# Performance work log

Hardware: AMD Instinct MI355X
Metric: run time of the kernel (lower is better)

The kernel has to match this reference:

```python
import jax, jax.numpy as jnp
from jax import lax
import numpy as np

B, H0, W0, C = 2, 192, 192, 192
CH = C // 2            # channels per attention branch (window / stripe)
D = 4                  # blocks in the stage
WS = 8                 # window / stripe size
NHW = 4                # window-attention heads
NHS = 4                # stripe-attention heads
ADF = 2                # anchor down factor (avgpool)
MLP_RATIO = 4

def _rel_pos_index(ws):
    coords = np.stack(np.meshgrid(np.arange(ws), np.arange(ws), indexing="ij"))
    coords = coords.reshape(2, -1)
    rel = coords[:, :, None] - coords[:, None, :]
    rel = rel.transpose(1, 2, 0) + (ws - 1)
    return rel[..., 0] * (2 * ws - 1) + rel[..., 1]

REL_IDX = jnp.asarray(_rel_pos_index(WS))  # [N, N] into (2*WS-1)^2 table

def _swin_mask(H, W, ws, shift):
    img = np.zeros((H, W))
    cnt = 0
    for hs in (slice(0, -ws), slice(-ws, -shift), slice(-shift, None)):
        for wsl in (slice(0, -ws), slice(-ws, -shift), slice(-shift, None)):
            img[hs, wsl] = cnt
            cnt += 1
    win = img.reshape(H // ws, ws, W // ws, ws).transpose(0, 2, 1, 3).reshape(-1, ws * ws)
    diff = win[:, None, :] - win[:, :, None]
    return jnp.asarray(np.where(diff != 0, -100.0, 0.0), jnp.float32)

def _ln(x, g, b):
    mu = x.mean(-1, keepdims=True)
    var = x.var(-1, keepdims=True)
    return (x - mu) * lax.rsqrt(var + 1e-5) * g + b

def _window_attn(xw, H, W, shift, qkv_w, qkv_b, rpb):
    Bb, L, Cw = xw.shape
    h, dh, N = NHW, Cw // NHW, WS * WS
    x = xw.reshape(Bb, H, W, Cw)
    if shift:
        x = jnp.roll(x, (-shift, -shift), (1, 2))
    nH, nW = H // WS, W // WS
    xw_ = x.reshape(Bb, nH, WS, nW, WS, Cw).transpose(0, 1, 3, 2, 4, 5).reshape(-1, N, Cw)
    qkv = (xw_ @ qkv_w + qkv_b).reshape(-1, N, 3, h, dh)
    q, k, v = qkv[:, :, 0], qkv[:, :, 1], qkv[:, :, 2]
    attn = jnp.einsum("wnhd,wmhd->whnm", q * dh ** -0.5, k)
    attn = attn + rpb[REL_IDX].transpose(2, 0, 1)[None]  # relative position bias [h,N,N]
    if shift:
        mask = _swin_mask(H, W, WS, shift)  # [nWin, N, N]
        attn = (attn.reshape(Bb, nH * nW, h, N, N) + mask[None, :, None]).reshape(-1, h, N, N)
    attn = jax.nn.softmax(attn, -1)
    out = jnp.einsum("whnm,wmhd->wnhd", attn, v).reshape(-1, N, Cw)
    x = out.reshape(Bb, nH, nW, WS, WS, Cw).transpose(0, 1, 3, 2, 4, 5).reshape(Bb, H, W, Cw)
    if shift:
        x = jnp.roll(x, (shift, shift), (1, 2))
    return x.reshape(Bb, L, Cw)

def _stripe_attn(xs, H, W, qkv_w, qkv_b):
    # anchored stripe attention: q -> anchors -> k/v (two small softmaxes)
    Bb, L, Cs = xs.shape
    h, dh, N = NHS, Cs // NHS, WS * WS
    M = (WS // ADF) * (WS // ADF)
    x = xs.reshape(Bb, H // WS, WS, W // WS, WS, Cs).transpose(0, 1, 3, 2, 4, 5)
    x = x.reshape(-1, WS, WS, Cs)
    anchor = x.reshape(-1, WS // ADF, ADF, WS // ADF, ADF, Cs).mean((2, 4)).reshape(-1, M, h, dh)
    xt = x.reshape(-1, N, Cs)
    qkv = (xt @ qkv_w + qkv_b).reshape(-1, N, 3, h, dh)
    q, k, v = qkv[:, :, 0], qkv[:, :, 1], qkv[:, :, 2]
    s = dh ** -0.5
    a1 = jax.nn.softmax(jnp.einsum("snhd,smhd->shnm", q * s, anchor), -1)  # [S,h,N,M]
    a2 = jax.nn.softmax(jnp.einsum("smhd,snhd->shmn", anchor * s, k), -1)  # [S,h,M,N]
    out = jnp.einsum("shnm,shmt,sthd->snhd", a1, a2, v).reshape(-1, N, Cs)
    out = out.reshape(Bb, H // WS, W // WS, WS, WS, Cs).transpose(0, 1, 3, 2, 4, 5)
    return out.reshape(Bb, L, Cs)

def setup_inputs() -> dict:
    key = jax.random.key(0)
    ks = jax.random.split(key, 8)
    std = 0.02
    return {
        "x": jax.random.normal(ks[0], (B, H0 * W0, C), jnp.float32),
        "norm1_g": jnp.ones((D, C), jnp.float32),
        "norm1_b": jnp.zeros((D, C), jnp.float32),
        "qkv_w_win": jax.random.normal(ks[1], (D, CH, 3 * CH), jnp.float32) * std,
        "qkv_b_win": jnp.zeros((D, 3 * CH), jnp.float32),
        "qkv_w_str": jax.random.normal(ks[2], (D, CH, 3 * CH), jnp.float32) * std,
        "qkv_b_str": jnp.zeros((D, 3 * CH), jnp.float32),
        "proj_w": jax.random.normal(ks[3], (D, C, C), jnp.float32) * std,
        "proj_b": jnp.zeros((D, C), jnp.float32),
        "rpb_table": jax.random.normal(ks[4], (D, (2 * WS - 1) ** 2, NHW), jnp.float32) * std,
        "norm2_g": jnp.ones((D, C), jnp.float32),
        "norm2_b": jnp.zeros((D, C), jnp.float32),
        "fc1_w": jax.random.normal(ks[5], (D, C, MLP_RATIO * C), jnp.float32) * std,
        "fc1_b": jnp.zeros((D, MLP_RATIO * C), jnp.float32),
        "fc2_w": jax.random.normal(ks[6], (D, MLP_RATIO * C, C), jnp.float32) * std,
        "fc2_b": jnp.zeros((D, C), jnp.float32),
        "conv_w": jax.random.normal(ks[7], (C, C, 3, 3), jnp.float32) * std,
        "conv_b": jnp.zeros((C,), jnp.float32),
        "H": H0,
        "W": W0,
    }

def reference(x, norm1_g, norm1_b, qkv_w_win, qkv_b_win, qkv_w_str, qkv_b_str,
              proj_w, proj_b, rpb_table, norm2_g, norm2_b, fc1_w, fc1_b,
              fc2_w, fc2_b, conv_w, conv_b, H, W):
    res0 = x
    for i in range(D):
        xn = _ln(x, norm1_g[i], norm1_b[i])
        shift = WS // 2 if i % 2 == 0 else 0  # window_shift = i % 2 == 0
        ow = _window_attn(xn[..., :CH], H, W, shift, qkv_w_win[i], qkv_b_win[i], rpb_table[i])
        os_ = _stripe_attn(xn[..., CH:], H, W, qkv_w_str[i], qkv_b_str[i])
        x = x + (jnp.concatenate([ow, os_], -1) @ proj_w[i] + proj_b[i])
        xn2 = _ln(x, norm2_g[i], norm2_b[i])
        x = x + (jax.nn.gelu(xn2 @ fc1_w[i] + fc1_b[i]) @ fc2_w[i] + fc2_b[i])
    Bb = x.shape[0]
    xc = x.reshape(Bb, H, W, C).transpose(0, 3, 1, 2)
    y = lax.conv_general_dilated(xc, conv_w, (1, 1), "SAME") + conv_b[None, :, None, None]
    y = y.transpose(0, 2, 3, 1).reshape(Bb, H * W, C)
    return y + res0  # long residual of the TransformerStage
```

## Files before the change

kernel.cpp:

```cpp
#include <hip/hip_runtime.h>
#include <math.h>

typedef __bf16 bf16_t;
typedef bf16_t bf16x8 __attribute__((ext_vector_type(8)));
typedef bf16_t bf16x4 __attribute__((ext_vector_type(4)));
typedef float f32x4 __attribute__((ext_vector_type(4)));

#define TOKS 73728
#define CCH 192

__device__ __forceinline__ float gelu_f(float x) {
  float x2 = x*x;
  float u = 1.5957691216057308f * x * fmaf(0.044715f, x2, 1.0f);
  float e = __expf(-u);
  return x * __builtin_amdgcn_rcpf(1.0f + e);
}

__device__ __forceinline__ void glds16(const void* g, void* l) {
  __builtin_amdgcn_global_load_lds(
      (const __attribute__((address_space(1))) void*)g,
      (__attribute__((address_space(3))) void*)l, 16, 0, 0);
}

__global__ void prep_all_k(const float* __restrict__ qw, const float* __restrict__ qs,
                           const float* __restrict__ pw, const float* __restrict__ f1,
                           const float* __restrict__ f2, const float* __restrict__ cw,
                           const float* __restrict__ rpb,
                           bf16_t* __restrict__ WwinT, bf16_t* __restrict__ WstrT,
                           bf16_t* __restrict__ WprojT, bf16_t* __restrict__ Wfc1T,
                           bf16_t* __restrict__ Wfc2T, bf16_t* __restrict__ WconvT,
                           float* __restrict__ RPB2) {
  long idx = (long)blockIdx.x*256 + threadIdx.x;
  auto tr = [](const float* in, bf16_t* out, long i, int K, int N) {
    long kn = (long)K*N;
    long c = i / kn;
    int rem = (int)(i - c*kn);
    int k = rem / N, n = rem % N;
    out[c*kn + (long)n*K + k] = (bf16_t)in[i];
  };
  if (idx < 110592)        tr(qw, WwinT, idx, 96, 288);
  else if (idx < 221184)   tr(qs, WstrT, idx-110592, 96, 288);
  else if (idx < 368640)   tr(pw, WprojT, idx-221184, 192, 192);
  else if (idx < 958464)   tr(f1, Wfc1T, idx-368640, 192, 768);
  else if (idx < 1548288)  tr(f2, Wfc2T, idx-958464, 768, 192);
  else if (idx < 1880064) {
    int i2 = (int)(idx - 1548288);
    int tap = i2 / 36864;
    int co = (i2 / 192) % 192;
    int ci = i2 % 192;
    WconvT[i2] = (bf16_t)cw[(co*192 + ci)*9 + tap];
  } else if (idx < 1945600) {
    int i2 = (int)(idx - 1880064);
    int i = i2 >> 14;
    int rem = i2 & 16383;
    int h = rem >> 12;
    int k = (rem >> 6) & 63;
    int c = (rem >> 2) & 15;
    int nt = rem & 3;
    int q = nt*16 + c;
    int ridx = ((q>>3) - (k>>3) + 7)*15 + ((q&7) - (k&7) + 7);
    RPB2[i2] = rpb[(i*225 + ridx)*4 + h];
  }
}

__global__ __launch_bounds__(256) void ln0_k(const float* __restrict__ x,
    const float* __restrict__ gg, const float* __restrict__ bb,
    bf16_t* __restrict__ out, float* __restrict__ xcopy) {
  const int wid = blockIdx.x*4 + (threadIdx.x >> 6);
  const int l = threadIdx.x & 63;
  const float* row = x + (long)wid*CCH;
  float v0 = row[l], v1 = row[l+64], v2 = row[l+128];
  float s = v0+v1+v2, s2 = v0*v0+v1*v1+v2*v2;
  #pragma unroll
  for (int off=1; off<64; off<<=1) { s += __shfl_xor(s, off); s2 += __shfl_xor(s2, off); }
  float mu = s * (1.f/CCH);
  float rstd = rsqrtf(s2*(1.f/CCH) - mu*mu + 1e-5f);
  float* crow = xcopy + (long)wid*CCH;
  crow[l] = v0; crow[l+64] = v1; crow[l+128] = v2;
  bf16_t* orow = out + (long)wid*CCH;
  orow[l]     = (bf16_t)((v0-mu)*rstd*gg[l]     + bb[l]);
  orow[l+64]  = (bf16_t)((v1-mu)*rstd*gg[l+64]  + bb[l+64]);
  orow[l+128] = (bf16_t)((v2-mu)*rstd*gg[l+128] + bb[l+128]);
}

template<int BK, int EPI>
__global__ __launch_bounds__(256) void gemma_k(
    const bf16_t* __restrict__ A, int lda,
    const bf16_t* __restrict__ Bt,
    const float* __restrict__ bias,
    bf16_t* __restrict__ outb, int ldo, int ooff, int K) {
  constexpr int NSLOT = BK/8;
  constexpr int MASK  = NSLOT-1;
  constexpr int KS    = BK/32;
  constexpr int RPS   = 512/BK;
  constexpr int SLA   = 128*BK/512;
  constexpr int SLB   = 96*BK/512;
  __shared__ bf16_t As[2][128*BK];
  __shared__ bf16_t Bs[2][96*BK];
  const int tid = threadIdx.x;
  const int w = tid >> 6, l = tid & 63;
  const int lr = l & 15, lk = l >> 4;
  const int ri = l / NSLOT, si = l & MASK;
  const long m0 = (long)blockIdx.x * 128;
  const int n0 = blockIdx.y * 96;
  const int wm = w >> 1, wn = w & 1;

  f32x4 acc[4][3];
  #pragma unroll
  for (int mi=0;mi<4;++mi)
    #pragma unroll
    for (int ni=0;ni<3;++ni) acc[mi][ni] = (f32x4){0.f,0.f,0.f,0.f};

  const int nk = K / BK;
  auto stage = [&](int buf, int k0) {
    #pragma unroll
    for (int j = 0; j < SLA/4; ++j) {
      const int s = j*4 + w;
      const int gr = s*RPS + ri;
      glds16(A + (m0+gr)*(long)lda + k0 + ((si ^ (gr&MASK))*8), &As[buf][s*512]);
    }
    #pragma unroll
    for (int j = 0; j < (SLB+3)/4; ++j) {
      const int s = j*4 + w;
      if (s < SLB) {
        const int gr = s*RPS + ri;
        glds16(Bt + (long)(n0+gr)*K + k0 + ((si ^ (gr&MASK))*8), &Bs[buf][s*512]);
      }
    }
  };

  stage(0, 0);
  __syncthreads();
  for (int kt = 0; kt < nk; ++kt) {
    const int cur = kt & 1;
    if (kt + 1 < nk) stage(cur^1, (kt+1)*BK);
    #pragma unroll
    for (int ks = 0; ks < KS; ++ks) {
      bf16x8 af[4], bfr[3];
      #pragma unroll
      for (int mi=0;mi<4;++mi) {
        const int ar = wm*64 + mi*16 + lr;
        const int slot = (ks*4 + lk) ^ (ar & MASK);
        af[mi] = *(const bf16x8*)(&As[cur][ar*BK + slot*8]);
      }
      #pragma unroll
      for (int ni=0;ni<3;++ni) {
        const int br = wn*48 + ni*16 + lr;
        const int slot = (ks*4 + lk) ^ (br & MASK);
        bfr[ni] = *(const bf16x8*)(&Bs[cur][br*BK + slot*8]);
      }
      #pragma unroll
      for (int mi=0;mi<4;++mi)
        #pragma unroll
        for (int ni=0;ni<3;++ni)
          acc[mi][ni] = __builtin_amdgcn_mfma_f32_16x16x32_bf16(af[mi], bfr[ni], acc[mi][ni], 0, 0, 0);
    }
    __syncthreads();
  }

  #pragma unroll
  for (int mi=0;mi<4;++mi) {
    const long r0 = m0 + wm*64 + mi*16 + lk*4;
    #pragma unroll
    for (int ni=0;ni<3;++ni) {
      const int col = n0 + wn*48 + ni*16 + lr;
      const float bs = bias[col];
      #pragma unroll
      for (int e=0;e<4;++e) {
        const float v = acc[mi][ni][e] + bs;
        const long row = r0 + e;
        outb[row*ldo + ooff + col] = (EPI==1) ? (bf16_t)gelu_f(v) : (bf16_t)v;
      }
    }
  }
}

__global__ __launch_bounds__(256) void gemmq_k(
    const bf16_t* __restrict__ xn,
    const bf16_t* __restrict__ BtW, const bf16_t* __restrict__ BtS,
    const float* __restrict__ biasW, const float* __restrict__ biasS,
    bf16_t* __restrict__ outb) {
  constexpr int BK=32, MASK=3, RPS=16;
  __shared__ bf16_t As[2][128*32];
  __shared__ bf16_t Bs[2][96*32];
  const int tid = threadIdx.x;
  const int w = tid >> 6, l = tid & 63;
  const int lr = l & 15, lk = l >> 4;
  const int ri = l >> 2, si = l & MASK;
  const long m0 = (long)blockIdx.x * 128;
  const bool iswin = blockIdx.y < 3;
  const int n0 = (iswin ? blockIdx.y : blockIdx.y - 3) * 96;
  const bf16_t* A = iswin ? xn : xn + 96;
  const bf16_t* Bt = iswin ? BtW : BtS;
  const float* bias = iswin ? biasW : biasS;
  const int ooff = iswin ? 0 : 288;
  const int wm = w >> 1, wn = w & 1;

  f32x4 acc[4][3];
  #pragma unroll
  for (int mi=0;mi<4;++mi)
    #pragma unroll
    for (int ni=0;ni<3;++ni) acc[mi][ni] = (f32x4){0.f,0.f,0.f,0.f};

  auto stage = [&](int buf, int k0) {
    #pragma unroll
    for (int j = 0; j < 2; ++j) {
      const int s = j*4 + w;
      const int gr = s*RPS + ri;
      glds16(A + (m0+gr)*192L + k0 + ((si ^ (gr&MASK))*8), &As[buf][s*512]);
    }
    #pragma unroll
    for (int j = 0; j < 2; ++j) {
      const int s = j*4 + w;
      if (s < 6) {
        const int gr = s*RPS + ri;
        glds16(Bt + (long)(n0+gr)*96 + k0 + ((si ^ (gr&MASK))*8), &Bs[buf][s*512]);
      }
    }
  };

  stage(0, 0);
  __syncthreads();
  for (int kt = 0; kt < 3; ++kt) {
    const int cur = kt & 1;
    if (kt + 1 < 3) stage(cur^1, (kt+1)*BK);
    bf16x8 af[4], bfr[3];
    #pragma unroll
    for (int mi=0;mi<4;++mi) {
      const int ar = wm*64 + mi*16 + lr;
      const int slot = lk ^ (ar & MASK);
      af[mi] = *(const bf16x8*)(&As[cur][ar*32 + slot*8]);
    }
    #pragma unroll
    for (int ni=0;ni<3;++ni) {
      const int br = wn*48 + ni*16 + lr;
      const int slot = lk ^ (br & MASK);
      bfr[ni] = *(const bf16x8*)(&Bs[cur][br*32 + slot*8]);
    }
    #pragma unroll
    for (int mi=0;mi<4;++mi)
      #pragma unroll
      for (int ni=0;ni<3;++ni)
        acc[mi][ni] = __builtin_amdgcn_mfma_f32_16x16x32_bf16(af[mi], bfr[ni], acc[mi][ni], 0, 0, 0);
    __syncthreads();
  }

  #pragma unroll
  for (int mi=0;mi<4;++mi) {
    const long r0 = m0 + wm*64 + mi*16 + lk*4;
    #pragma unroll
    for (int ni=0;ni<3;++ni) {
      const int col = n0 + wn*48 + ni*16 + lr;
      const float bs = bias[col];
      #pragma unroll
      for (int e=0;e<4;++e) {
        const long row = r0 + e;
        outb[row*576 + ooff + col] = (bf16_t)(acc[mi][ni][e] + bs);
      }
    }
  }
}

template<int EPI>
__global__ __launch_bounds__(512) void gemmb_k(
    const bf16_t* __restrict__ A,
    const bf16_t* __restrict__ Bt,
    const float* __restrict__ bias,
    float* __restrict__ resid,
    bf16_t* __restrict__ xnout,
    const float* __restrict__ gg, const float* __restrict__ bb,
    int K) {
  constexpr int BK=64, MASK=7;
  __shared__ bf16_t As[2][128*64];
  __shared__ bf16_t Bs[2][192*64];
  const int tid = threadIdx.x;
  const int w = tid >> 6, l = tid & 63;
  const int lr = l & 15, lk = l >> 4;
  const int ri = l >> 3, si = l & 7;
  const int wm = w >> 2, wn = w & 3;
  const long m0 = (long)blockIdx.x * 128;

  f32x4 acc[4][3];
  #pragma unroll
  for (int mi=0;mi<4;++mi)
    #pragma unroll
    for (int ni=0;ni<3;++ni) acc[mi][ni] = (f32x4){0.f,0.f,0.f,0.f};

  const int nk = K / BK;
  auto stage = [&](int buf, int k0) {
    #pragma unroll
    for (int j = 0; j < 2; ++j) {
      const int s = j*8 + w;
      const int gr = s*8 + ri;
      glds16(A + (m0+gr)*(long)K + k0 + ((si ^ (gr&MASK))*8), &As[buf][s*512]);
    }
    #pragma unroll
    for (int j = 0; j < 3; ++j) {
      const int s = j*8 + w;
      const int gr = s*8 + ri;
      glds16(Bt + (long)gr*K + k0 + ((si ^ (gr&MASK))*8), &Bs[buf][s*512]);
    }
  };

  stage(0, 0);
  __syncthreads();
  for (int kt = 0; kt < nk; ++kt) {
    const int cur = kt & 1;
    if (kt + 1 < nk) stage(cur^1, (kt+1)*BK);
    #pragma unroll
    for (int ks = 0; ks < 2; ++ks) {
      bf16x8 af[4], bfr[3];
      #pragma unroll
      for (int mi=0;mi<4;++mi) {
        const int ar = wm*64 + mi*16 + lr;
        const int slot = (ks*4 + lk) ^ (ar & MASK);
        af[mi] = *(const bf16x8*)(&As[cur][ar*64 + slot*8]);
      }
      #pragma unroll
      for (int ni=0;ni<3;++ni) {
        const int br = wn*48 + ni*16 + lr;
        const int slot = (ks*4 + lk) ^ (br & MASK);
        bfr[ni] = *(const bf16x8*)(&Bs[cur][br*64 + slot*8]);
      }
      #pragma unroll
      for (int mi=0;mi<4;++mi)
        #pragma unroll
        for (int ni=0;ni<3;++ni)
          acc[mi][ni] = __builtin_amdgcn_mfma_f32_16x16x32_bf16(af[mi], bfr[ni], acc[mi][ni], 0, 0, 0);
    }
    __syncthreads();
  }

  #pragma unroll
  for (int mi=0;mi<4;++mi) {
    #pragma unroll
    for (int ni=0;ni<3;++ni) {
      const int col = wn*48 + ni*16 + lr;
      const float bs = bias[col];
      #pragma unroll
      for (int e=0;e<4;++e) {
        const long row = m0 + wm*64 + mi*16 + lk*4 + e;
        float v = acc[mi][ni][e] + bs + resid[row*CCH + col];
        acc[mi][ni][e] = v;
        resid[row*CCH + col] = v;
        if (EPI == 1) xnout[row*CCH + col] = (bf16_t)v;
      }
    }
  }
  if (EPI == 0) {
    float* red  = (float*)&As[0][0];
    float* stat = red + 1024;
    #pragma unroll
    for (int mi=0;mi<4;++mi) {
      #pragma unroll
      for (int e=0;e<4;++e) {
        float p1 = acc[mi][0][e] + acc[mi][1][e] + acc[mi][2][e];
        float p2 = acc[mi][0][e]*acc[mi][0][e] + acc[mi][1][e]*acc[mi][1][e]
                 + acc[mi][2][e]*acc[mi][2][e];
        #pragma unroll
        for (int off=1; off<16; off<<=1) {
          p1 += __shfl_xor(p1, off);
          p2 += __shfl_xor(p2, off);
        }
        if (lr == 0) {
          const int r = wm*64 + mi*16 + lk*4 + e;
          red[(r*4 + wn)*2]     = p1;
          red[(r*4 + wn)*2 + 1] = p2;
        }
      }
    }
    __syncthreads();
    if (tid < 128) {
      const int r = tid;
      float s1 = red[(r*4+0)*2] + red[(r*4+1)*2] + red[(r*4+2)*2] + red[(r*4+3)*2];
      float s2 = red[(r*4+0)*2+1] + red[(r*4+1)*2+1] + red[(r*4+2)*2+1] + red[(r*4+3)*2+1];
      const float mu = s1 * (1.f/CCH);
      stat[r*2]   = mu;
      stat[r*2+1] = rsqrtf(s2*(1.f/CCH) - mu*mu + 1e-5f);
    }
    __syncthreads();
    #pragma unroll
    for (int mi=0;mi<4;++mi) {
      #pragma unroll
      for (int e=0;e<4;++e) {
        const int r = wm*64 + mi*16 + lk*4 + e;
        const float mu = stat[r*2], rstd = stat[r*2+1];
        #pragma unroll
        for (int ni=0;ni<3;++ni) {
          const int col = wn*48 + ni*16 + lr;
          xnout[(m0+r)*CCH + col] = (bf16_t)((acc[mi][ni][e]-mu)*rstd*gg[col] + bb[col]);
        }
      }
    }
  }
}

__global__ __launch_bounds__(256) void win_attn3_k(
    const bf16_t* __restrict__ qkv, bf16_t* __restrict__ aout,
    const float* __restrict__ rpb2, int shift) {
  __shared__ bf16_t Vs[4][64][28];
  __shared__ bf16_t Pl[4][64][68];
  __shared__ float invl[4][64];
  const int h = threadIdx.x >> 6, l = threadIdx.x & 63;
  const int c = l & 15, g = l >> 4;
  const int wblk = blockIdx.x;
  const int b = wblk / 576, wi = wblk % 576;
  const int wh = wi / 24, ww = wi % 24;

  auto gtok = [&](int t) -> long {
    int ho = wh*8 + (t>>3) + shift; if (ho >= 192) ho -= 192;
    int wo = ww*8 + (t&7) + shift;  if (wo >= 192) wo -= 192;
    return (long)b*36864 + (long)ho*192 + wo;
  };

  {
    const bf16_t* vsrc = qkv + gtok(l)*576 + 192 + h*24;
    #pragma unroll
    for (int j=0;j<3;++j) {
      bf16x4 lo = *(const bf16x4*)(vsrc + j*8);
      bf16x4 hi = *(const bf16x4*)(vsrc + j*8 + 4);
      *(bf16x4*)(&Vs[h][l][j*8])   = lo;
      *(bf16x4*)(&Vs[h][l][j*8+4]) = hi;
    }
    *(bf16x4*)(&Vs[h][l][24]) = (bf16x4){};
  }

  bf16x8 kf[4], qf[4];
  #pragma unroll
  for (int t=0;t<4;++t) {
    bf16x8 z = {};
    kf[t] = z; qf[t] = z;
    if (g < 3) {
      const bf16_t* pb = qkv + gtok(16*t + c)*576 + h*24 + g*8;
      qf[t] = *(const bf16x8*)(pb);
      kf[t] = *(const bf16x8*)(pb + 96);
    }
  }

  f32x4 st[4][4];
  #pragma unroll
  for (int mt=0;mt<4;++mt)
    #pragma unroll
    for (int nt=0;nt<4;++nt)
      st[mt][nt] = __builtin_amdgcn_mfma_f32_16x16x32_bf16(kf[mt], qf[nt], (f32x4){0.f,0.f,0.f,0.f}, 0, 0, 0);

  const float scale = 0.20412414523193154f;
  const float4* rp = (const float4*)rpb2 + (h*64*16 + c);
  #pragma unroll
  for (int mt=0;mt<4;++mt) {
    #pragma unroll
    for (int r=0;r<4;++r) {
      const int k = 16*mt + 4*g + r;
      float4 b4 = rp[k*16];
      st[mt][0][r] = fmaf(st[mt][0][r], scale, b4.x);
      st[mt][1][r] = fmaf(st[mt][1][r], scale, b4.y);
      st[mt][2][r] = fmaf(st[mt][2][r], scale, b4.z);
      st[mt][3][r] = fmaf(st[mt][3][r], scale, b4.w);
    }
  }

  if (shift && (wh==23 || ww==23)) {
    #pragma unroll
    for (int mt=0;mt<4;++mt)
      #pragma unroll
      for (int r=0;r<4;++r) {
        const int kk = 16*mt + 4*g + r;
        const int krc = (wh==23) ? (((kk>>3)<4)?1:2) : 0;
        const int kcc = (ww==23) ? (((kk&7)<4)?1:2) : 0;
        const int kcls = krc*3 + kcc;
        #pragma unroll
        for (int nt=0;nt<4;++nt) {
          const int qq = 16*nt + c;
          const int qrc = (wh==23) ? (((qq>>3)<4)?1:2) : 0;
          const int qcc = (ww==23) ? (((qq&7)<4)?1:2) : 0;
          if (qrc*3 + qcc != kcls) st[mt][nt][r] -= 100.f;
        }
      }
  }

  #pragma unroll
  for (int nt=0;nt<4;++nt) {
    float m = st[0][nt][0];
    #pragma unroll
    for (int mt=0;mt<4;++mt)
      #pragma unroll
      for (int r=0;r<4;++r) m = fmaxf(m, st[mt][nt][r]);
    m = fmaxf(m, __shfl_xor(m, 16));
    m = fmaxf(m, __shfl_xor(m, 32));
    float s = 0.f;
    #pragma unroll
    for (int mt=0;mt<4;++mt)
      #pragma unroll
      for (int r=0;r<4;++r) {
        float p = __expf(st[mt][nt][r] - m);
        st[mt][nt][r] = p;
        s += p;
      }
    s += __shfl_xor(s, 16);
    s += __shfl_xor(s, 32);
    if (g == 0) invl[h][16*nt + c] = 1.f / s;
  }

  #pragma unroll
  for (int mt=0;mt<4;++mt) {
    #pragma unroll
    for (int nt=0;nt<4;++nt) {
      const int q = 16*nt + c;
      const int sl = (4*mt + g) ^ ((q&7)<<1);
      bf16x4 pk;
      #pragma unroll
      for (int r=0;r<4;++r) pk[r] = (bf16_t)st[mt][nt][r];
      *(bf16x4*)(&Pl[h][q][sl*4]) = pk;
    }
  }

  f32x4 oa[4][2];
  #pragma unroll
  for (int mt=0;mt<4;++mt)
    #pragma unroll
    for (int nt=0;nt<2;++nt) oa[mt][nt] = (f32x4){0.f,0.f,0.f,0.f};

  #pragma unroll
  for (int s2=0;s2<2;++s2) {
    bf16x8 pfr[4];
    #pragma unroll
    for (int mt=0;mt<4;++mt) {
      const int q = 16*mt + c;
      const int S0 = (8*s2 + 2*g) ^ ((q&7)<<1);
      bf16x4 lo = *(const bf16x4*)(&Pl[h][q][S0*4]);
      bf16x4 hi = *(const bf16x4*)(&Pl[h][q][S0*4 + 4]);
      #pragma unroll
      for (int r=0;r<4;++r) { pfr[mt][r] = lo[r]; pfr[mt][4+r] = hi[r]; }
    }
    #pragma unroll
    for (int nt=0;nt<2;++nt) {
      const int d = 16*nt + c;
      const int deff = (d < 24) ? d : 24;
      bf16x8 vf;
      #pragma unroll
      for (int e=0;e<8;++e) vf[e] = Vs[h][32*s2 + 8*g + e][deff];
      #pragma unroll
      for (int mt=0;mt<4;++mt)
        oa[mt][nt] = __builtin_amdgcn_mfma_f32_16x16x32_bf16(pfr[mt], vf, oa[mt][nt], 0, 0, 0);
    }
  }

  #pragma unroll
  for (int mt=0;mt<4;++mt) {
    #pragma unroll
    for (int r=0;r<4;++r) {
      const int q = 16*mt + 4*g + r;
      const float inv = invl[h][q];
      bf16_t* ob = aout + gtok(q)*192 + h*24;
      #pragma unroll
      for (int nt=0;nt<2;++nt) {
        const int d = 16*nt + c;
        if (d < 24) ob[d] = (bf16_t)(oa[mt][nt][r] * inv);
      }
    }
  }
}

__global__ __launch_bounds__(256) void stripe_attn3_k(
    const bf16_t* __restrict__ qkv, const bf16_t* __restrict__ xn,
    bf16_t* __restrict__ aout) {
  __shared__ bf16_t Vs[4][64][28];
  __shared__ bf16_t Ans[4][16][40];
  __shared__ bf16_t a2s[4][16][68];
  __shared__ bf16_t a1s[4][64][24];
  __shared__ bf16_t Ts2[4][32][28];
  const int h = threadIdx.x >> 6, l = threadIdx.x & 63;
  const int c = l & 15, g = l >> 4;
  const int wblk = blockIdx.x;
  const int b = wblk / 576, wi = wblk % 576;
  const int wh = wi / 24, ww = wi % 24;
  const long base0 = (long)b*36864 + (long)(wh*8)*192 + ww*8;
  auto gtok = [&](int t) -> long { return base0 + (long)(t>>3)*192 + (t&7); };

  {
    const bf16_t* vsrc = qkv + gtok(l)*576 + 480 + h*24;
    #pragma unroll
    for (int j=0;j<3;++j) {
      *(bf16x4*)(&Vs[h][l][j*8])   = *(const bf16x4*)(vsrc + j*8);
      *(bf16x4*)(&Vs[h][l][j*8+4]) = *(const bf16x4*)(vsrc + j*8 + 4);
    }
    *(bf16x4*)(&Vs[h][l][24]) = (bf16x4){};
  }
  {
    const int m = l >> 2, dq = l & 3;
    const int ar = m >> 2, ac = m & 3;
    const bf16_t* t0 = xn + (base0 + (long)(2*ar)*192 + 2*ac)*192 + 96 + h*24;
    #pragma unroll
    for (int j=0;j<6;++j) {
      const int d = dq*6 + j;
      float ssum = (float)t0[d] + (float)t0[192+d] + (float)t0[36864+d] + (float)t0[37056+d];
      Ans[h][m][d] = (bf16_t)(0.25f*ssum);
    }
  }
  if (l < 16) {
    *(bf16x4*)(&Ans[h][l][24]) = (bf16x4){};
    *(bf16x4*)(&Ans[h][l][28]) = (bf16x4){};
    bf16_t* z = &Ts2[h][16+l][0];
    #pragma unroll
    for (int j=0;j<7;++j) *(bf16x4*)(z + j*4) = (bf16x4){};
    *(bf16x4*)(&Ts2[h][l][24]) = (bf16x4){};
  }

  bf16x8 anf = *(const bf16x8*)(&Ans[h][c][g*8]);

  bf16x8 kf[4], qf[4];
  #pragma unroll
  for (int t=0;t<4;++t) {
    const bf16_t* pb = qkv + gtok(16*t + c)*576 + 288 + h*24 + g*8;
    qf[t] = *(const bf16x8*)(pb);
    kf[t] = *(const bf16x8*)(pb + 96);
  }

  const float scale = 0.20412414523193154f;

  f32x4 st2[4];
  #pragma unroll
  for (int mt=0;mt<4;++mt)
    st2[mt] = __builtin_amdgcn_mfma_f32_16x16x32_bf16(kf[mt], anf, (f32x4){0.f,0.f,0.f,0.f}, 0, 0, 0);

  {
    float m2 = -1e30f;
    #pragma unroll
    for (int mt=0;mt<4;++mt)
      #pragma unroll
      for (int r=0;r<4;++r) { st2[mt][r] *= scale; m2 = fmaxf(m2, st2[mt][r]); }
    m2 = fmaxf(m2, __shfl_xor(m2, 16));
    m2 = fmaxf(m2, __shfl_xor(m2, 32));
    float s = 0.f;
    #pragma unroll
    for (int mt=0;mt<4;++mt)
      #pragma unroll
      for (int r=0;r<4;++r) { float p = __expf(st2[mt][r] - m2); st2[mt][r] = p; s += p; }
    s += __shfl_xor(s, 16);
    s += __shfl_xor(s, 32);
    const float inv = 1.f / s;
    #pragma unroll
    for (int mt=0;mt<4;++mt) {
      const int sl = (4*mt + g) ^ ((c&7)<<1);
      bf16x4 pk;
      #pragma unroll
      for (int r=0;r<4;++r) pk[r] = (bf16_t)(st2[mt][r] * inv);
      *(bf16x4*)(&a2s[h][c][sl*4]) = pk;
    }
  }

  f32x4 ta[2];
  ta[0] = (f32x4){0.f,0.f,0.f,0.f}; ta[1] = (f32x4){0.f,0.f,0.f,0.f};
  #pragma unroll
  for (int kt=0;kt<2;++kt) {
    const int S0 = (8*kt + 2*g) ^ ((c&7)<<1);
    bf16x4 lo = *(const bf16x4*)(&a2s[h][c][S0*4]);
    bf16x4 hi = *(const bf16x4*)(&a2s[h][c][S0*4 + 4]);
    bf16x8 pf;
    #pragma unroll
    for (int r=0;r<4;++r) { pf[r] = lo[r]; pf[4+r] = hi[r]; }
    #pragma unroll
    for (int nt2=0;nt2<2;++nt2) {
      const int d = 16*nt2 + c;
      const int deff = (d < 24) ? d : 24;
      bf16x8 vf;
      #pragma unroll
      for (int e=0;e<8;++e) vf[e] = Vs[h][kt*32 + 8*g + e][deff];
      ta[nt2] = __builtin_amdgcn_mfma_f32_16x16x32_bf16(pf, vf, ta[nt2], 0, 0, 0);
    }
  }
  #pragma unroll
  for (int nt2=0;nt2<2;++nt2) {
    const int d = 16*nt2 + c;
    if (d < 24) {
      #pragma unroll
      for (int r=0;r<4;++r) Ts2[h][4*g + r][d] = (bf16_t)ta[nt2][r];
    }
  }

  f32x4 st1[4];
  #pragma unroll
  for (int nt=0;nt<4;++nt)
    st1[nt] = __builtin_amdgcn_mfma_f32_16x16x32_bf16(anf, qf[nt], (f32x4){0.f,0.f,0.f,0.f}, 0, 0, 0);

  #pragma unroll
  for (int nt=0;nt<4;++nt) {
    float m1 = -1e30f;
    #pragma unroll
    for (int r=0;r<4;++r) { st1[nt][r] *= scale; m1 = fmaxf(m1, st1[nt][r]); }
    m1 = fmaxf(m1, __shfl_xor(m1, 16));
    m1 = fmaxf(m1, __shfl_xor(m1, 32));
    float s = 0.f;
    #pragma unroll
    for (int r=0;r<4;++r) { float p = __expf(st1[nt][r] - m1); st1[nt][r] = p; s += p; }
    s += __shfl_xor(s, 16);
    s += __shfl_xor(s, 32);
    const float inv1 = 1.f / s;
    bf16x4 ak;
    #pragma unroll
    for (int r=0;r<4;++r) ak[r] = (bf16_t)(st1[nt][r] * inv1);
    *(bf16x4*)(&a1s[h][16*nt + c][4*g]) = ak;
  }

  f32x4 oa[4][2];
  #pragma unroll
  for (int mt=0;mt<4;++mt) { oa[mt][0] = (f32x4){0.f,0.f,0.f,0.f}; oa[mt][1] = (f32x4){0.f,0.f,0.f,0.f}; }
  #pragma unroll
  for (int mt=0;mt<4;++mt) {
    bf16x8 af = {};
    if (g < 2) af = *(const bf16x8*)(&a1s[h][16*mt + c][g*8]);
    #pragma unroll
    for (int nt2=0;nt2<2;++nt2) {
      const int d = 16*nt2 + c;
      const int deff = (d < 24) ? d : 24;
      bf16x8 tf;
      #pragma unroll
      for (int e=0;e<8;++e) tf[e] = Ts2[h][8*g + e][deff];
      oa[mt][nt2] = __builtin_amdgcn_mfma_f32_16x16x32_bf16(af, tf, oa[mt][nt2], 0, 0, 0);
    }
  }

  #pragma unroll
  for (int mt=0;mt<4;++mt) {
    #pragma unroll
    for (int r=0;r<4;++r) {
      const int tw = 16*mt + 4*g + r;
      bf16_t* ob = aout + gtok(tw)*192 + 96 + h*24;
      #pragma unroll
      for (int nt2=0;nt2<2;++nt2) {
        const int d = 16*nt2 + c;
        if (d < 24) ob[d] = (bf16_t)(oa[mt][nt2][r]);
      }
    }
  }
}

__global__ __launch_bounds__(256) void conv3_k(
    const bf16_t* __restrict__ xb,
    const bf16_t* __restrict__ Wc,
    const float* __restrict__ cb,
    const float* __restrict__ res0,
    const bf16_t* __restrict__ zb,
    float* __restrict__ out) {
  __shared__ bf16_t Xs[19968];
  __shared__ bf16_t Bs[18432];
  const int tid = threadIdx.x;
  const int w = tid >> 6, l = tid & 63;
  const int lr = l & 15, lk = l >> 4;
  const int rq = l >> 2, cq = (l & 3) * 8;
  const int bxr = blockIdx.x;
  const int bx = (bxr & 7) * 48 + (bxr >> 3);
  const int bimg = bx / 192, h = bx % 192;
  const int co0 = blockIdx.y * 64;

  f32x4 acc[3][4];
  #pragma unroll
  for (int mi=0; mi<3; ++mi)
    #pragma unroll
    for (int ni=0; ni<4; ++ni) acc[mi][ni] = (f32x4){0.f,0.f,0.f,0.f};

  for (int kcs = 0; kcs < 6; ++kcs) {
    const int kc = kcs * 32;
    for (int j = 0; j < 10; ++j) {
      int s = j*4 + w;
      if (s < 39) {
        int dy = s / 13, rem = s - dy*13;
        int tokcol = rem*16 + rq;
        int wc = tokcol - 1;
        int hp = h + dy - 1;
        const bf16_t* src = zb + cq;
        if (hp >= 0 && hp < 192 && wc >= 0 && wc < 192)
          src = xb + ((long)bimg*36864 + (long)hp*192 + wc)*192 + kc + cq;
        glds16(src, &Xs[s*512]);
      }
    }
    for (int j = 0; j < 9; ++j) {
      int s = j*4 + w;
      int tap = s >> 2, rem = s & 3;
      int row = rem*16 + rq;
      glds16(Wc + ((long)(tap*192 + co0 + row))*192 + kc + cq, &Bs[s*512]);
    }
    __syncthreads();
    #pragma unroll
    for (int tap = 0; tap < 9; ++tap) {
      const int dy = tap/3, dx = tap%3 - 1;
      bf16x8 af[3];
      #pragma unroll
      for (int mi=0; mi<3; ++mi) {
        int tokcol = w*48 + mi*16 + lr + dx + 1;
        af[mi] = *(const bf16x8*)(&Xs[dy*6656 + tokcol*32 + lk*8]);
      }
      #pragma unroll
      for (int ni=0; ni<4; ++ni) {
        bf16x8 bfr = *(const bf16x8*)(&Bs[tap*2048 + (ni*16+lr)*32 + lk*8]);
        #pragma unroll
        for (int mi=0; mi<3; ++mi)
          acc[mi][ni] = __builtin_amdgcn_mfma_f32_16x16x32_bf16(af[mi], bfr, acc[mi][ni], 0, 0, 0);
      }
    }
    if (kcs < 5) __syncthreads();
  }

  #pragma unroll
  for (int mi=0; mi<3; ++mi) {
    #pragma unroll
    for (int ni=0; ni<4; ++ni) {
      const int col = co0 + ni*16 + lr;
      const float cbv = cb[col];
      #pragma unroll
      for (int e=0; e<4; ++e) {
        const int tl = w*48 + mi*16 + lk*4 + e;
        const long tok = (long)bimg*36864 + (long)h*192 + tl;
        out[tok*192 + col] = acc[mi][ni][e] + cbv + res0[tok*192 + col];
      }
    }
  }
}

extern "C" void kernel_launch(void* const* d_in, const int* in_sizes, int n_in,
                              void* d_out, int out_size, void* d_ws, size_t ws_size,
                              hipStream_t stream) {
  const float* x_in     = (const float*)d_in[0];
  const float* norm1_g  = (const float*)d_in[1];
  const float* norm1_b  = (const float*)d_in[2];
  const float* qkv_w_w  = (const float*)d_in[3];
  const float* qkv_b_w  = (const float*)d_in[4];
  const float* qkv_w_s  = (const float*)d_in[5];
  const float* qkv_b_s  = (const float*)d_in[6];
  const float* proj_w   = (const float*)d_in[7];
  const float* proj_b   = (const float*)d_in[8];
  const float* rpb      = (const float*)d_in[9];
  const float* norm2_g  = (const float*)d_in[10];
  const float* norm2_b  = (const float*)d_in[11];
  const float* fc1_w    = (const float*)d_in[12];
  const float* fc1_b    = (const float*)d_in[13];
  const float* fc2_w    = (const float*)d_in[14];
  const float* fc2_b    = (const float*)d_in[15];
  const float* conv_w   = (const float*)d_in[16];
  const float* conv_b   = (const float*)d_in[17];

  char* ws = (char*)d_ws;
  float*  x_cur = (float*)ws;
  bf16_t* xn    = (bf16_t*)(ws + 56623104);
  bf16_t* qh    = (bf16_t*)(ws + 84934656);
  bf16_t* aoutb = (bf16_t*)(ws + 198180864);
  bf16_t* WwinT = (bf16_t*)(ws + 226492416);
  bf16_t* WstrT  = WwinT  + 110592;
  bf16_t* WprojT = WstrT  + 110592;
  bf16_t* Wfc1T  = WprojT + 147456;
  bf16_t* Wfc2T  = Wfc1T  + 589824;
  bf16_t* WconvT = Wfc2T  + 589824;
  float*  RPB2   = (float*)(WconvT + 331776);

  prep_all_k<<<7600, 256, 0, stream>>>(qkv_w_w, qkv_w_s, proj_w, fc1_w, fc2_w,
                                       conv_w, rpb,
                                       WwinT, WstrT, WprojT, Wfc1T, Wfc2T, WconvT, RPB2);

  ln0_k<<<TOKS/4, 256, 0, stream>>>(x_in, norm1_g, norm1_b, xn, x_cur);

  const int MB = TOKS/128;
  for (int i = 0; i < 4; ++i) {
    int shift = (i % 2 == 0) ? 4 : 0;
    dim3 g6(MB, 6), g8(MB, 8);
    gemmq_k<<<g6, 256, 0, stream>>>(xn, WwinT + (long)i*27648, WstrT + (long)i*27648,
                                    qkv_b_w + i*288, qkv_b_s + i*288, qh);
    win_attn3_k<<<1152, 256, 0, stream>>>(qh, aoutb, RPB2 + i*16384, shift);
    stripe_attn3_k<<<1152, 256, 0, stream>>>(qh, xn, aoutb);
    gemmb_k<0><<<MB, 512, 0, stream>>>(aoutb, WprojT + (long)i*36864, proj_b + i*192,
                                       x_cur, xn, norm2_g + i*192, norm2_b + i*192, 192);
    gemma_k<32,1><<<g8, 256, 0, stream>>>(xn, 192, Wfc1T + (long)i*147456, fc1_b + i*768,
                                          qh, 768, 0, 192);
    if (i < 3)
      gemmb_k<0><<<MB, 512, 0, stream>>>(qh, Wfc2T + (long)i*147456, fc2_b + i*192,
                                         x_cur, xn, norm1_g + (i+1)*192, norm1_b + (i+1)*192, 768);
    else
      gemmb_k<1><<<MB, 512, 0, stream>>>(qh, Wfc2T + (long)i*147456, fc2_b + i*192,
                                         x_cur, aoutb, nullptr, nullptr, 768);
  }
  hipMemsetAsync(qh, 0, 4096, stream);
  dim3 gc(384, 3);
  conv3_k<<<gc, 256, 0, stream>>>(aoutb, WconvT, conv_b, x_in, qh, (float*)d_out);
}
```

Before: 1.028 ms.

## Fuse fc1+GELU+fc2 MLP into one kernel keeping hidden activations in LDS

Replaces the separate fc1 GEMM (which wrote the 768-wide GELU hidden tensor to global memory) and the fc2 GEMM with a single mlp_k kernel. Each 128-row block loops over 8 hidden chunks of 96, computes fc1+GELU into shared memory, and immediately accumulates into fc2, followed by the same residual/LayerNorm epilogue. This removes a large global write/read of the hidden activations and one launch per block. In exchange it uses about 147KB of LDS per block, which limits occupancy, and the weights are reloaded per chunk with no double buffering.

```diff
diff --git a/kernel.cpp b/kernel.cpp
--- a/kernel.cpp
+++ b/kernel.cpp
@@ -83,98 +83,6 @@
   orow[l+128] = (bf16_t)((v2-mu)*rstd*gg[l+128] + bb[l+128]);
 }
 
-template<int BK, int EPI>
-__global__ __launch_bounds__(256) void gemma_k(
-    const bf16_t* __restrict__ A, int lda,
-    const bf16_t* __restrict__ Bt,
-    const float* __restrict__ bias,
-    bf16_t* __restrict__ outb, int ldo, int ooff, int K) {
-  constexpr int NSLOT = BK/8;
-  constexpr int MASK  = NSLOT-1;
-  constexpr int KS    = BK/32;
-  constexpr int RPS   = 512/BK;
-  constexpr int SLA   = 128*BK/512;
-  constexpr int SLB   = 96*BK/512;
-  __shared__ bf16_t As[2][128*BK];
-  __shared__ bf16_t Bs[2][96*BK];
-  const int tid = threadIdx.x;
-  const int w = tid >> 6, l = tid & 63;
-  const int lr = l & 15, lk = l >> 4;
-  const int ri = l / NSLOT, si = l & MASK;
-  const long m0 = (long)blockIdx.x * 128;
-  const int n0 = blockIdx.y * 96;
-  const int wm = w >> 1, wn = w & 1;
-
-  f32x4 acc[4][3];
-  #pragma unroll
-  for (int mi=0;mi<4;++mi)
-    #pragma unroll
-    for (int ni=0;ni<3;++ni) acc[mi][ni] = (f32x4){0.f,0.f,0.f,0.f};
-
-  const int nk = K / BK;
-  auto stage = [&](int buf, int k0) {
-    #pragma unroll
-    for (int j = 0; j < SLA/4; ++j) {
-      const int s = j*4 + w;
-      const int gr = s*RPS + ri;
-      glds16(A + (m0+gr)*(long)lda + k0 + ((si ^ (gr&MASK))*8), &As[buf][s*512]);
-    }
-    #pragma unroll
-    for (int j = 0; j < (SLB+3)/4; ++j) {
-      const int s = j*4 + w;
-      if (s < SLB) {
-        const int gr = s*RPS + ri;
-        glds16(Bt + (long)(n0+gr)*K + k0 + ((si ^ (gr&MASK))*8), &Bs[buf][s*512]);
-      }
-    }
-  };
-
-  stage(0, 0);
-  __syncthreads();
-  for (int kt = 0; kt < nk; ++kt) {
-    const int cur = kt & 1;
-    if (kt + 1 < nk) stage(cur^1, (kt+1)*BK);
-    #pragma unroll
-    for (int ks = 0; ks < KS; ++ks) {
-      bf16x8 af[4], bfr[3];
-      #pragma unroll
-      for (int mi=0;mi<4;++mi) {
-        const int ar = wm*64 + mi*16 + lr;
-        const int slot = (ks*4 + lk) ^ (ar & MASK);
-        af[mi] = *(const bf16x8*)(&As[cur][ar*BK + slot*8]);
-      }
-      #pragma unroll
-      for (int ni=0;ni<3;++ni) {
-        const int br = wn*48 + ni*16 + lr;
-        const int slot = (ks*4 + lk) ^ (br & MASK);
-        bfr[ni] = *(const bf16x8*)(&Bs[cur][br*BK + slot*8]);
-      }
-      #pragma unroll
-      for (int mi=0;mi<4;++mi)
-        #pragma unroll
-        for (int ni=0;ni<3;++ni)
-          acc[mi][ni] = __builtin_amdgcn_mfma_f32_16x16x32_bf16(af[mi], bfr[ni], acc[mi][ni], 0, 0, 0);
-    }
-    __syncthreads();
-  }
-
-  #pragma unroll
-  for (int mi=0;mi<4;++mi) {
-    const long r0 = m0 + wm*64 + mi*16 + lk*4;
-    #pragma unroll
-    for (int ni=0;ni<3;++ni) {
-      const int col = n0 + wn*48 + ni*16 + lr;
-      const float bs = bias[col];
-      #pragma unroll
-      for (int e=0;e<4;++e) {
-        const float v = acc[mi][ni][e] + bs;
-        const long row = r0 + e;
-        outb[row*ldo + ooff + col] = (EPI==1) ? (bf16_t)gelu_f(v) : (bf16_t)v;
-      }
-    }
-  }
-}
-
 __global__ __launch_bounds__(256) void gemmq_k(
     const bf16_t* __restrict__ xn,
     const bf16_t* __restrict__ BtW, const bf16_t* __restrict__ BtS,
@@ -349,6 +257,191 @@
   }
   if (EPI == 0) {
     float* red  = (float*)&As[0][0];
+    float* stat = red + 1024;
+    #pragma unroll
+    for (int mi=0;mi<4;++mi) {
+      #pragma unroll
+      for (int e=0;e<4;++e) {
+        float p1 = acc[mi][0][e] + acc[mi][1][e] + acc[mi][2][e];
+        float p2 = acc[mi][0][e]*acc[mi][0][e] + acc[mi][1][e]*acc[mi][1][e]
+                 + acc[mi][2][e]*acc[mi][2][e];
+        #pragma unroll
+        for (int off=1; off<16; off<<=1) {
+          p1 += __shfl_xor(p1, off);
+          p2 += __shfl_xor(p2, off);
+        }
+        if (lr == 0) {
+          const int r = wm*64 + mi*16 + lk*4 + e;
+          red[(r*4 + wn)*2]     = p1;
+          red[(r*4 + wn)*2 + 1] = p2;
+        }
+      }
+    }
+    __syncthreads();
+    if (tid < 128) {
+      const int r = tid;
+      float s1 = red[(r*4+0)*2] + red[(r*4+1)*2] + red[(r*4+2)*2] + red[(r*4+3)*2];
+      float s2 = red[(r*4+0)*2+1] + red[(r*4+1)*2+1] + red[(r*4+2)*2+1] + red[(r*4+3)*2+1];
+      const float mu = s1 * (1.f/CCH);
+      stat[r*2]   = mu;
+      stat[r*2+1] = rsqrtf(s2*(1.f/CCH) - mu*mu + 1e-5f);
+    }
+    __syncthreads();
+    #pragma unroll
+    for (int mi=0;mi<4;++mi) {
+      #pragma unroll
+      for (int e=0;e<4;++e) {
+        const int r = wm*64 + mi*16 + lk*4 + e;
+        const float mu = stat[r*2], rstd = stat[r*2+1];
+        #pragma unroll
+        for (int ni=0;ni<3;++ni) {
+          const int col = wn*48 + ni*16 + lr;
+          xnout[(m0+r)*CCH + col] = (bf16_t)((acc[mi][ni][e]-mu)*rstd*gg[col] + bb[col]);
+        }
+      }
+    }
+  }
+}
+
+template<int EPI>
+__global__ __launch_bounds__(512) void mlp_k(
+    const bf16_t* __restrict__ xnin,
+    const bf16_t* __restrict__ W1T,
+    const float* __restrict__ b1,
+    const bf16_t* __restrict__ W2T,
+    const float* __restrict__ b2,
+    float* __restrict__ resid,
+    bf16_t* __restrict__ xnout,
+    const float* __restrict__ gg, const float* __restrict__ bb) {
+  __shared__ __attribute__((aligned(16))) char smem[150528];
+  bf16_t* Xs  = (bf16_t*)smem;
+  bf16_t* Hs  = (bf16_t*)(smem + 49152);
+  bf16_t* W1s = (bf16_t*)(smem + 73728);
+  bf16_t* W2s = (bf16_t*)(smem + 110592);
+  float*  B1s = (float*)(smem + 147456);
+  const int tid = threadIdx.x;
+  const int w = tid >> 6, l = tid & 63;
+  const int lr = l & 15, lk = l >> 4;
+  const int rq = l >> 2, si = l & 3;
+  const int wm = w >> 2, wn = w & 3;
+  const int w1m = w >> 1, w1n = w & 1;
+  const long m0 = (long)blockIdx.x * 128;
+
+  for (int t = tid; t < 768; t += 512) B1s[t] = b1[t];
+  #pragma unroll
+  for (int j = 0; j < 6; ++j) {
+    const int s = j*8 + w;
+    const int kc = s >> 3;
+    const int row = (s & 7)*16 + rq;
+    glds16(xnin + (m0+row)*192 + kc*32 + ((si ^ (row&3))*8), (bf16_t*)smem + s*512);
+  }
+
+  f32x4 acc[4][3];
+  #pragma unroll
+  for (int mi=0;mi<4;++mi)
+    #pragma unroll
+    for (int ni=0;ni<3;++ni) acc[mi][ni] = (f32x4){0.f,0.f,0.f,0.f};
+
+  for (int hc = 0; hc < 8; ++hc) {
+    __syncthreads();
+    #pragma unroll
+    for (int j = 0; j < 5; ++j) {
+      const int s = j*8 + w;
+      if (s < 36) {
+        const int kc = s/6, rs = s - kc*6;
+        const int row = rs*16 + rq;
+        glds16(W1T + (long)(hc*96 + row)*192 + kc*32 + ((si ^ (row&3))*8), W1s + s*512);
+      }
+    }
+    #pragma unroll
+    for (int j = 0; j < 5; ++j) {
+      const int s = j*8 + w;
+      if (s < 36) {
+        const int kc = s/12, rs = s - kc*12;
+        const int row = rs*16 + rq;
+        glds16(W2T + (long)row*768 + hc*96 + kc*32 + ((si ^ (row&3))*8), W2s + s*512);
+      }
+    }
+    __syncthreads();
+    f32x4 ah[2][3];
+    #pragma unroll
+    for (int mi=0;mi<2;++mi)
+      #pragma unroll
+      for (int ni=0;ni<3;++ni) ah[mi][ni] = (f32x4){0.f,0.f,0.f,0.f};
+    #pragma unroll
+    for (int kc = 0; kc < 6; ++kc) {
+      bf16x8 af[2], bfr[3];
+      #pragma unroll
+      for (int mi=0;mi<2;++mi) {
+        const int ar = w1m*32 + mi*16 + lr;
+        af[mi] = *(const bf16x8*)(Xs + kc*4096 + ar*32 + ((lk ^ (ar&3))*8));
+      }
+      #pragma unroll
+      for (int ni=0;ni<3;++ni) {
+        const int br = w1n*48 + ni*16 + lr;
+        bfr[ni] = *(const bf16x8*)(W1s + kc*3072 + br*32 + ((lk ^ (br&3))*8));
+      }
+      #pragma unroll
+      for (int mi=0;mi<2;++mi)
+        #pragma unroll
+        for (int ni=0;ni<3;++ni)
+          ah[mi][ni] = __builtin_amdgcn_mfma_f32_16x16x32_bf16(af[mi], bfr[ni], ah[mi][ni], 0, 0, 0);
+    }
+    #pragma unroll
+    for (int mi=0;mi<2;++mi) {
+      #pragma unroll
+      for (int ni=0;ni<3;++ni) {
+        const int col = w1n*48 + ni*16 + lr;
+        const int kc2 = col >> 5, ch = col & 31;
+        const int sil = ch >> 3, cho = ch & 7;
+        const float bs = B1s[hc*96 + col];
+        #pragma unroll
+        for (int e=0;e<4;++e) {
+          const int r = w1m*32 + mi*16 + lk*4 + e;
+          Hs[kc2*4096 + r*32 + ((sil ^ (r&3))<<3) + cho] = (bf16_t)gelu_f(ah[mi][ni][e] + bs);
+        }
+      }
+    }
+    __syncthreads();
+    #pragma unroll
+    for (int kc = 0; kc < 3; ++kc) {
+      bf16x8 af[4], bfr[3];
+      #pragma unroll
+      for (int mi=0;mi<4;++mi) {
+        const int ar = wm*64 + mi*16 + lr;
+        af[mi] = *(const bf16x8*)(Hs + kc*4096 + ar*32 + ((lk ^ (ar&3))*8));
+      }
+      #pragma unroll
+      for (int ni=0;ni<3;++ni) {
+        const int br = wn*48 + ni*16 + lr;
+        bfr[ni] = *(const bf16x8*)(W2s + kc*6144 + br*32 + ((lk ^ (br&3))*8));
+      }
+      #pragma unroll
+      for (int mi=0;mi<4;++mi)
+        #pragma unroll
+        for (int ni=0;ni<3;++ni)
+          acc[mi][ni] = __builtin_amdgcn_mfma_f32_16x16x32_bf16(af[mi], bfr[ni], acc[mi][ni], 0, 0, 0);
+    }
+  }
+
+  #pragma unroll
+  for (int mi=0;mi<4;++mi) {
+    #pragma unroll
+    for (int ni=0;ni<3;++ni) {
+      const int col = wn*48 + ni*16 + lr;
+      const float bs = b2[col];
+      #pragma unroll
+      for (int e=0;e<4;++e) {
+        const long row = m0 + wm*64 + mi*16 + lk*4 + e;
+        float v = acc[mi][ni][e] + bs + resid[row*CCH + col];
+        acc[mi][ni][e] = v;
+        resid[row*CCH + col] = v;
+        if (EPI == 1) xnout[row*CCH + col] = (bf16_t)v;
+      }
+    }
+  }
+  if (EPI == 0) {
+    float* red  = (float*)smem;
     float* stat = red + 1024;
     #pragma unroll
     for (int mi=0;mi<4;++mi) {
@@ -861,21 +954,21 @@
   const int MB = TOKS/128;
   for (int i = 0; i < 4; ++i) {
     int shift = (i % 2 == 0) ? 4 : 0;
-    dim3 g6(MB, 6), g8(MB, 8);
+    dim3 g6(MB, 6);
     gemmq_k<<<g6, 256, 0, stream>>>(xn, WwinT + (long)i*27648, WstrT + (long)i*27648,
                                     qkv_b_w + i*288, qkv_b_s + i*288, qh);
     win_attn3_k<<<1152, 256, 0, stream>>>(qh, aoutb, RPB2 + i*16384, shift);
     stripe_attn3_k<<<1152, 256, 0, stream>>>(qh, xn, aoutb);
     gemmb_k<0><<<MB, 512, 0, stream>>>(aoutb, WprojT + (long)i*36864, proj_b + i*192,
                                        x_cur, xn, norm2_g + i*192, norm2_b + i*192, 192);
-    gemma_k<32,1><<<g8, 256, 0, stream>>>(xn, 192, Wfc1T + (long)i*147456, fc1_b + i*768,
-                                          qh, 768, 0, 192);
     if (i < 3)
-      gemmb_k<0><<<MB, 512, 0, stream>>>(qh, Wfc2T + (long)i*147456, fc2_b + i*192,
-                                         x_cur, xn, norm1_g + (i+1)*192, norm1_b + (i+1)*192, 768);
+      mlp_k<0><<<MB, 512, 0, stream>>>(xn, Wfc1T + (long)i*147456, fc1_b + i*768,
+                                       Wfc2T + (long)i*147456, fc2_b + i*192,
+                                       x_cur, xn, norm1_g + (i+1)*192, norm1_b + (i+1)*192);
     else
-      gemmb_k<1><<<MB, 512, 0, stream>>>(qh, Wfc2T + (long)i*147456, fc2_b + i*192,
-                                         x_cur, aoutb, nullptr, nullptr, 768);
+      mlp_k<1><<<MB, 512, 0, stream>>>(xn, Wfc1T + (long)i*147456, fc1_b + i*768,
+                                       Wfc2T + (long)i*147456, fc2_b + i*192,
+                                       x_cur, aoutb, nullptr, nullptr);
   }
   hipMemsetAsync(qh, 0, 4096, stream);
   dim3 gc(384, 3);
```

Result: slower. 1.101 ms (+7.1%).
